# Optimization experiments

Hardware: AMD Instinct MI355X
Metric: run time of the kernel (lower is better)

The kernel has to match this reference:

```python
import jax, jax.numpy as jnp
import numpy as np

EPS = 1e-5
NUM_HEADS = 4


def setup_inputs() -> dict:
    key = jax.random.key(0)
    ks = jax.random.split(key, 6)
    B, C, H, W = 16, 256, 32, 32
    x = jax.random.normal(ks[0], (B, C, H, W), dtype=jnp.float32)
    gamma = jnp.ones((C,), jnp.float32)
    beta = jnp.zeros((C,), jnp.float32)
    run_mean = jax.random.normal(ks[1], (C,), dtype=jnp.float32) * 0.1
    run_var = jax.random.uniform(ks[2], (C,), dtype=jnp.float32, minval=0.5, maxval=1.5)
    qkv_w = jax.random.normal(ks[3], (3 * C, C), dtype=jnp.float32) * (1.0 / np.sqrt(C))
    qkv_b = jnp.zeros((3 * C,), jnp.float32)
    out_w = jax.random.normal(ks[4], (C, C), dtype=jnp.float32) * (1.0 / np.sqrt(C))
    out_b = jnp.zeros((C,), jnp.float32)
    return {"x": x, "gamma": gamma, "beta": beta, "run_mean": run_mean,
            "run_var": run_var, "qkv_w": qkv_w, "qkv_b": qkv_b,
            "out_w": out_w, "out_b": out_b}


def reference(x, gamma, beta, run_mean, run_var, qkv_w, qkv_b, out_w, out_b):
    B, C, H, W = x.shape
    n = NUM_HEADS
    hd = C // n
    # BatchNorm2d (eval mode, running stats)
    inv = jax.lax.rsqrt(run_var + EPS)
    xn = (x - run_mean[:, None, None]) * (inv * gamma)[:, None, None] + beta[:, None, None]
    # 1x1 conv -> QKV: [B, 3C, H, W]
    qkv = jnp.einsum('oc,bchw->bohw', qkv_w, xn) + qkv_b[:, None, None]
    qkv = qkv.reshape(B, n, 3 * hd, H, W)
    q, k, v = qkv[:, :, :hd], qkv[:, :, hd:2 * hd], qkv[:, :, 2 * hd:]
    # full spatial attention; note scale is sqrt(C), per source
    attn = jnp.einsum('bnchw,bncyx->bnhwyx', q, k) / jnp.sqrt(jnp.float32(C))
    attn = jax.nn.softmax(attn.reshape(B, n, H, W, H * W), axis=-1)
    attn = attn.reshape(B, n, H, W, H, W)
    av = jnp.einsum('bnhwyx,bncyx->bnchw', attn, v).reshape(B, C, H, W)
    out = jnp.einsum('oc,bchw->bohw', out_w, av) + out_b[:, None, None]
    return x + out
```

## Files before the change

kernel.cpp:

```cpp
#include <hip/hip_runtime.h>
#include <hip/hip_bf16.h>

__device__ __forceinline__ float bf2f(unsigned short u) {
    return __uint_as_float(((unsigned int)u) << 16);
}
__device__ __forceinline__ unsigned short f2bf(float f) {
    unsigned int u = __float_as_uint(f);
    unsigned int r = (u + 0x7fffu + ((u >> 16) & 1u)) >> 16;
    return (unsigned short)r;
}
__device__ __forceinline__ float ld1(const void* p, long i, bool isf32) {
    return isf32 ? ((const float*)p)[i] : bf2f(((const unsigned short*)p)[i]);
}

typedef __attribute__((ext_vector_type(8))) short bh8;
typedef __attribute__((ext_vector_type(4))) float f32x4;

#define MFMA(a, b, c) __builtin_amdgcn_mfma_f32_16x16x32_bf16(a, b, c, 0, 0, 0)

#define S_TOK 1024
#define C_DIM 256
#define O_QKV 768
#define HD    64
#define NREG  196608
#define QOFF  0
#define KOFF  65536
#define VOFF  131072

__global__ __launch_bounds__(256) void prep_kernel(
    const void* __restrict__ gamma, const void* __restrict__ beta,
    const void* __restrict__ rmean, const void* __restrict__ rvar,
    const void* __restrict__ qkv_w, const void* __restrict__ qkv_b,
    const void* __restrict__ out_w, const void* __restrict__ out_b,
    unsigned short* __restrict__ w1b, float* __restrict__ b1,
    unsigned short* __restrict__ w2b, float* __restrict__ b2,
    int* __restrict__ flg)
{
    const unsigned g0 = *(const unsigned*)gamma;
    const bool isf32 = (g0 == 0x3F800000u);
    const int t   = threadIdx.x;
    const int blk = blockIdx.x;
    if (blk == 0 && t == 0) flg[0] = isf32 ? 1 : 0;
    if (blk < O_QKV) {
        const int c = t, o = blk;
        const float v  = ld1(rvar, c, isf32);
        const float a  = ld1(gamma, c, isf32) * rsqrtf(fmaxf(v, 0.f) + 1e-5f);
        const float sh = ld1(beta, c, isf32) - ld1(rmean, c, isf32) * a;
        const float w  = ld1(qkv_w, (long)o * C_DIM + c, isf32);
        w1b[(size_t)o * C_DIM + c] = f2bf(w * a);
        __shared__ float red[256];
        red[c] = w * sh;
        __syncthreads();
        for (int st = 128; st > 0; st >>= 1) {
            if (c < st) red[c] += red[c + st];
            __syncthreads();
        }
        if (c == 0) b1[o] = ld1(qkv_b, o, isf32) + red[0];
    } else {
        const int c = t, o = blk - O_QKV;
        w2b[(size_t)o * C_DIM + c] = f2bf(ld1(out_w, (long)o * C_DIM + c, isf32));
        if (c == 0) b2[o] = ld1(out_b, o, isf32);
    }
}

__global__ __launch_bounds__(256) void gemm_qkv_kernel(
    const unsigned short* __restrict__ w1b, const float* __restrict__ b1,
    const void* __restrict__ x, unsigned short* __restrict__ qkv,
    int b0, const int* __restrict__ flg)
{
    const bool isf32 = (flg[0] != 0);
    const int s0 = blockIdx.x * 64;
    const int oh = blockIdx.y;
    const int z  = blockIdx.z;
    const int b  = b0 + z;
    const int t  = threadIdx.x;
    const int wave = t >> 6, lane = t & 63;
    const int quad = lane >> 4, l16 = lane & 15;

    __shared__ unsigned short xs[64 * 266];

    const size_t xbase = (size_t)b * C_DIM * S_TOK + s0 + lane;
#pragma unroll 4
    for (int it = 0; it < 64; ++it) {
        const int ci = it * 4 + wave;
        const float v = ld1(x, xbase + (size_t)ci * S_TOK, isf32);
        xs[lane * 266 + ci] = f2bf(v);
    }
    __syncthreads();

#pragma unroll 1
    for (int ot = 0; ot < 6; ++ot) {
        const int o0 = (oh * 6 + ot) * 64;
        const int ow = o0 + wave * 16 + l16;
        bh8 af[8];
#pragma unroll
        for (int kc = 0; kc < 8; ++kc)
            af[kc] = *(const bh8*)&w1b[(size_t)ow * C_DIM + kc * 32 + quad * 8];

        f32x4 acc[4];
#pragma unroll
        for (int nt = 0; nt < 4; ++nt) acc[nt] = (f32x4){0.f, 0.f, 0.f, 0.f};
#pragma unroll
        for (int kc = 0; kc < 8; ++kc) {
#pragma unroll
            for (int nt = 0; nt < 4; ++nt) {
                const bh8 bf = *(const bh8*)&xs[(nt * 16 + l16) * 266 + kc * 32 + quad * 8];
                acc[nt] = MFMA(af[kc], bf, acc[nt]);
            }
        }
        const int n      = o0 / 192;
        const int region = (o0 >> 6) % 3;
        const int och    = wave * 16 + quad * 4;
        float bias_r[4];
#pragma unroll
        for (int r = 0; r < 4; ++r) bias_r[r] = b1[o0 + och + r];
        unsigned short* hb = qkv + (size_t)z * O_QKV * S_TOK + n * NREG;
        if (region < 2) {
            const float sc = (region == 0) ? 0.0625f : 1.0f;
            unsigned short* qb = hb + (region == 0 ? QOFF : KOFF);
#pragma unroll
            for (int nt = 0; nt < 4; ++nt) {
                const int tk = s0 + nt * 16 + l16;
                ushort4 rr;
                rr.x = f2bf((acc[nt][0] + bias_r[0]) * sc);
                rr.y = f2bf((acc[nt][1] + bias_r[1]) * sc);
                rr.z = f2bf((acc[nt][2] + bias_r[2]) * sc);
                rr.w = f2bf((acc[nt][3] + bias_r[3]) * sc);
                *(ushort4*)&qb[(size_t)tk * 64 + och] = rr;
            }
        } else {
            unsigned short* vb = hb + VOFF;
#pragma unroll
            for (int nt = 0; nt < 4; ++nt) {
                const int tk = s0 + nt * 16 + l16;
#pragma unroll
                for (int r = 0; r < 4; ++r)
                    vb[(size_t)(och + r) * S_TOK + tk] = f2bf(acc[nt][r] + bias_r[r]);
            }
        }
    }
}

__global__ __launch_bounds__(256, 4) void attn_mfma_kernel(
    const unsigned short* __restrict__ qkv, unsigned short* __restrict__ avT)
{
    const int n  = blockIdx.x & 3;
    const int z  = blockIdx.x >> 2;
    const int qt = blockIdx.y;
    const int q0 = qt * 64;
    const int t  = threadIdx.x;
    const int wave = t >> 6, lane = t & 63;
    const int quad = lane >> 4, l16 = lane & 15;

    const unsigned short* qtp = qkv + (size_t)z * O_QKV * S_TOK + n * NREG + QOFF;
    const unsigned short* ktp = qtp + KOFF;
    const unsigned short* vcp = qtp + VOFF;

    __shared__ unsigned short p_lds[64 * 72];
    __shared__ float rs_lds[64 * 4];

    bh8 qf[4][2];
#pragma unroll
    for (int qs = 0; qs < 4; ++qs) {
        const size_t qrow = (size_t)(q0 + qs * 16 + l16) * 64;
        qf[qs][0] = *(const bh8*)&qtp[qrow + quad * 8];
        qf[qs][1] = *(const bh8*)&qtp[qrow + 32 + quad * 8];
    }

    f32x4 oacc[4];
#pragma unroll
    for (int i = 0; i < 4; ++i) oacc[i] = (f32x4){0.f, 0.f, 0.f, 0.f};
    float rs[4][4];
#pragma unroll
    for (int qs = 0; qs < 4; ++qs)
#pragma unroll
        for (int r = 0; r < 4; ++r) rs[qs][r] = 0.f;

    for (int chunk = 0; chunk < 16; ++chunk) {
        const int c0 = chunk * 64;
        const size_t krow = (size_t)(c0 + wave * 16 + l16) * 64;
        const bh8 kf0 = *(const bh8*)&ktp[krow + quad * 8];
        const bh8 kf1 = *(const bh8*)&ktp[krow + 32 + quad * 8];
        const size_t vrow = (size_t)(wave * 16 + l16) * S_TOK + c0;
        const bh8 vf0 = *(const bh8*)&vcp[vrow + quad * 8];
        const bh8 vf1 = *(const bh8*)&vcp[vrow + 32 + quad * 8];

        f32x4 sacc[4];
#pragma unroll
        for (int qs = 0; qs < 4; ++qs) {
            f32x4 a = (f32x4){0.f, 0.f, 0.f, 0.f};
            a = MFMA(qf[qs][0], kf0, a);
            a = MFMA(qf[qs][1], kf1, a);
            sacc[qs] = a;
        }
        __syncthreads();
#pragma unroll
        for (int qs = 0; qs < 4; ++qs) {
#pragma unroll
            for (int r = 0; r < 4; ++r) {
                const float p = __expf(sacc[qs][r] - 8.0f);
                rs[qs][r] += p;
                p_lds[(qs * 16 + quad * 4 + r) * 72 + wave * 16 + l16] =
                    (unsigned short)(__float_as_uint(p) >> 16);
            }
        }
        __syncthreads();
#pragma unroll
        for (int qs = 0; qs < 4; ++qs) {
            const bh8 pf0 = *(const bh8*)&p_lds[(qs * 16 + l16) * 72 + quad * 8];
            const bh8 pf1 = *(const bh8*)&p_lds[(qs * 16 + l16) * 72 + 32 + quad * 8];
            oacc[qs] = MFMA(pf0, vf0, oacc[qs]);
            oacc[qs] = MFMA(pf1, vf1, oacc[qs]);
        }
    }
#pragma unroll
    for (int off = 1; off < 16; off <<= 1) {
#pragma unroll
        for (int qs = 0; qs < 4; ++qs)
#pragma unroll
            for (int r = 0; r < 4; ++r) rs[qs][r] += __shfl_xor(rs[qs][r], off);
    }
    if (l16 == 0) {
#pragma unroll
        for (int qs = 0; qs < 4; ++qs)
#pragma unroll
            for (int r = 0; r < 4; ++r)
                rs_lds[(qs * 16 + quad * 4 + r) * 4 + wave] = rs[qs][r];
    }
    __syncthreads();
    const int ch = wave * 16 + l16;
#pragma unroll
    for (int qs = 0; qs < 4; ++qs) {
#pragma unroll
        for (int r = 0; r < 4; ++r) {
            const int q = qs * 16 + quad * 4 + r;
            const float4 rw = *(const float4*)&rs_lds[q * 4];
            const float inv = 1.0f / (rw.x + rw.y + rw.z + rw.w);
            p_lds[q * 72 + ch] = f2bf(oacc[qs][r] * inv);
        }
    }
    __syncthreads();
    const int tok = t >> 2, cq = t & 3;
    const uint4 w0 = *(const uint4*)&p_lds[tok * 72 + cq * 16];
    const uint4 w1 = *(const uint4*)&p_lds[tok * 72 + cq * 16 + 8];
    unsigned short* dst = avT + (((size_t)z << 10) + q0 + tok) * C_DIM + n * HD + cq * 16;
    *(uint4*)dst = w0;
    *(uint4*)(dst + 8) = w1;
}

__global__ __launch_bounds__(256) void gemm_out_kernel(
    const unsigned short* __restrict__ w2b, const float* __restrict__ b2,
    const void* __restrict__ x, const unsigned short* __restrict__ avT,
    void* __restrict__ out, int b0, const int* __restrict__ flg)
{
    const bool isf32 = (flg[0] != 0);
    const int s0 = blockIdx.x * 64;
    const int o0 = blockIdx.y * 64;
    const int z  = blockIdx.z;
    const int b  = b0 + z;
    const int t  = threadIdx.x;
    const int wave = t >> 6, lane = t & 63;
    const int quad = lane >> 4, l16 = lane & 15;

    __shared__ unsigned short vs_lds[64 * 258];

    const unsigned short* ab = avT + (((size_t)z << 10) + s0) * C_DIM;
#pragma unroll
    for (int it = 0; it < 8; ++it) {
        const int idx = it * 256 + t;
        const int tok = idx >> 5, c = (idx & 31) * 8;
        const bh8 v = *(const bh8*)&ab[tok * C_DIM + c];
        const ushort4* vp = (const ushort4*)&v;
        *(ushort4*)&vs_lds[tok * 258 + c]     = vp[0];
        *(ushort4*)&vs_lds[tok * 258 + c + 4] = vp[1];
    }
    const int ow = o0 + wave * 16 + l16;
    bh8 af[8];
#pragma unroll
    for (int kc = 0; kc < 8; ++kc)
        af[kc] = *(const bh8*)&w2b[(size_t)ow * C_DIM + kc * 32 + quad * 8];
    __syncthreads();

    f32x4 acc[4];
#pragma unroll
    for (int nt = 0; nt < 4; ++nt) acc[nt] = (f32x4){0.f, 0.f, 0.f, 0.f};
#pragma unroll
    for (int kc = 0; kc < 8; ++kc) {
#pragma unroll
        for (int nt = 0; nt < 4; ++nt) {
            const bh8 bf = *(const bh8*)&vs_lds[(nt * 16 + l16) * 258 + kc * 32 + quad * 8];
            acc[nt] = MFMA(af[kc], bf, acc[nt]);
        }
    }
    const int obase = o0 + wave * 16 + quad * 4;
    float bias_r[4];
#pragma unroll
    for (int r = 0; r < 4; ++r) bias_r[r] = b2[obase + r];
#pragma unroll
    for (int nt = 0; nt < 4; ++nt) {
        const int tk = s0 + nt * 16 + l16;
#pragma unroll
        for (int r = 0; r < 4; ++r) {
            const size_t base = ((size_t)b * C_DIM + obase + r) * S_TOK + tk;
            if (isf32) {
                ((float*)out)[base] = acc[nt][r] + bias_r[r] + ((const float*)x)[base];
            } else {
                ((unsigned short*)out)[base] =
                    f2bf(acc[nt][r] + bias_r[r] + bf2f(((const unsigned short*)x)[base]));
            }
        }
    }
}

extern "C" void kernel_launch(void* const* d_in, const int* in_sizes, int n_in,
                              void* d_out, int out_size, void* d_ws, size_t ws_size,
                              hipStream_t stream)
{
    const void* x     = d_in[0];
    const void* gamma = d_in[1];
    const void* beta  = d_in[2];
    const void* rmean = d_in[3];
    const void* rvar  = d_in[4];
    const void* qkv_w = d_in[5];
    const void* qkv_b = d_in[6];
    const void* out_w = d_in[7];
    const void* out_b = d_in[8];

    unsigned short* w1b = (unsigned short*)d_ws;
    unsigned short* w2b = w1b + 768 * 256;
    float* b1 = (float*)(w2b + 256 * 256);
    float* b2 = b1 + 768;
    int*   flg = (int*)(b2 + 256);
    const size_t fixed_bytes = (768 * 256 + 256 * 256) * 2 + (768 + 256) * 4 + 16;
    const size_t per_b = (size_t)(768 * 1024 + 256 * 1024) * 2;

    long long avail = (long long)ws_size - (long long)fixed_bytes;
    int G = (avail > 0) ? (int)(avail / (long long)per_b) : 1;
    if (G < 1) G = 1;
    if (G > 16) G = 16;
    if (G > 1) G &= ~1;

    unsigned short* qkv = (unsigned short*)((char*)d_ws + fixed_bytes);
    unsigned short* avT = qkv + (size_t)G * 768 * 1024;

    prep_kernel<<<1024, 256, 0, stream>>>(gamma, beta, rmean, rvar, qkv_w, qkv_b,
                                          out_w, out_b, w1b, b1, w2b, b2, flg);
    for (int b0 = 0; b0 < 16; b0 += G) {
        const int gb = (16 - b0 < G) ? (16 - b0) : G;
        gemm_qkv_kernel<<<dim3(16, 2, gb), 256, 0, stream>>>(w1b, b1, x, qkv, b0, flg);
        attn_mfma_kernel<<<dim3(4 * gb, 16, 1), 256, 0, stream>>>(qkv, avT);
        gemm_out_kernel<<<dim3(16, 4, gb), 256, 0, stream>>>(w2b, b2, x, avT, d_out, b0, flg);
    }
}
```

Before: 172.1 us.

## Write attention output in place over Q, vectorize x staging, prioritize MFMA waves

The attention kernel now writes its normalized output over the Q rows it already consumed, instead of a separate avT buffer. The output GEMM reads from that per-head layout, which drops the extra workspace and may allow a larger batch group per launch. The QKV GEMM now stages x with float4 (or 8-wide bf16) coalesced loads, with a tighter LDS row stride. s_setprio raises wave priority around the MFMA sections of the attention loop. Risks are more LDS bank conflicts from the transposed scalar stores and a dependence on each block reading only its own Q tile before overwriting it.

```diff
diff --git a/kernel.cpp b/kernel.cpp
--- a/kernel.cpp
+++ b/kernel.cpp
@@ -77,14 +77,32 @@
     const int wave = t >> 6, lane = t & 63;
     const int quad = lane >> 4, l16 = lane & 15;
 
-    __shared__ unsigned short xs[64 * 266];
-
-    const size_t xbase = (size_t)b * C_DIM * S_TOK + s0 + lane;
-#pragma unroll 4
-    for (int it = 0; it < 64; ++it) {
-        const int ci = it * 4 + wave;
-        const float v = ld1(x, xbase + (size_t)ci * S_TOK, isf32);
-        xs[lane * 266 + ci] = f2bf(v);
+    __shared__ unsigned short xs[64 * 258];
+
+    if (isf32) {
+        const float* xp = (const float*)x + (size_t)b * C_DIM * S_TOK + s0;
+#pragma unroll
+        for (int it = 0; it < 16; ++it) {
+            const int g  = it * 256 + t;
+            const int ch = g >> 4, tg = (g & 15) * 4;
+            const float4 v = *(const float4*)&xp[(size_t)ch * S_TOK + tg];
+            xs[(tg    ) * 258 + ch] = f2bf(v.x);
+            xs[(tg + 1) * 258 + ch] = f2bf(v.y);
+            xs[(tg + 2) * 258 + ch] = f2bf(v.z);
+            xs[(tg + 3) * 258 + ch] = f2bf(v.w);
+        }
+    } else {
+        const unsigned short* xp = (const unsigned short*)x + (size_t)b * C_DIM * S_TOK + s0;
+#pragma unroll
+        for (int it = 0; it < 8; ++it) {
+            const int g  = it * 256 + t;
+            const int ch = g >> 3, tg = (g & 7) * 8;
+            const bh8 v = *(const bh8*)&xp[(size_t)ch * S_TOK + tg];
+            const unsigned short* vs = (const unsigned short*)&v;
+#pragma unroll
+            for (int j = 0; j < 8; ++j)
+                xs[(tg + j) * 258 + ch] = vs[j];
+        }
     }
     __syncthreads();
 
@@ -104,7 +122,7 @@
         for (int kc = 0; kc < 8; ++kc) {
 #pragma unroll
             for (int nt = 0; nt < 4; ++nt) {
-                const bh8 bf = *(const bh8*)&xs[(nt * 16 + l16) * 266 + kc * 32 + quad * 8];
+                const bh8 bf = *(const bh8*)&xs[(nt * 16 + l16) * 258 + kc * 32 + quad * 8];
                 acc[nt] = MFMA(af[kc], bf, acc[nt]);
             }
         }
@@ -141,8 +159,7 @@
     }
 }
 
-__global__ __launch_bounds__(256, 4) void attn_mfma_kernel(
-    const unsigned short* __restrict__ qkv, unsigned short* __restrict__ avT)
+__global__ __launch_bounds__(256, 4) void attn_mfma_kernel(unsigned short* __restrict__ qkv)
 {
     const int n  = blockIdx.x & 3;
     const int z  = blockIdx.x >> 2;
@@ -152,7 +169,7 @@
     const int wave = t >> 6, lane = t & 63;
     const int quad = lane >> 4, l16 = lane & 15;
 
-    const unsigned short* qtp = qkv + (size_t)z * O_QKV * S_TOK + n * NREG + QOFF;
+    unsigned short* qtp = qkv + (size_t)z * O_QKV * S_TOK + n * NREG + QOFF;
     const unsigned short* ktp = qtp + KOFF;
     const unsigned short* vcp = qtp + VOFF;
 
@@ -186,6 +203,7 @@
         const bh8 vf1 = *(const bh8*)&vcp[vrow + 32 + quad * 8];
 
         f32x4 sacc[4];
+        __builtin_amdgcn_s_setprio(1);
 #pragma unroll
         for (int qs = 0; qs < 4; ++qs) {
             f32x4 a = (f32x4){0.f, 0.f, 0.f, 0.f};
@@ -193,6 +211,7 @@
             a = MFMA(qf[qs][1], kf1, a);
             sacc[qs] = a;
         }
+        __builtin_amdgcn_s_setprio(0);
         __syncthreads();
 #pragma unroll
         for (int qs = 0; qs < 4; ++qs) {
@@ -205,6 +224,7 @@
             }
         }
         __syncthreads();
+        __builtin_amdgcn_s_setprio(1);
 #pragma unroll
         for (int qs = 0; qs < 4; ++qs) {
             const bh8 pf0 = *(const bh8*)&p_lds[(qs * 16 + l16) * 72 + quad * 8];
@@ -212,6 +232,7 @@
             oacc[qs] = MFMA(pf0, vf0, oacc[qs]);
             oacc[qs] = MFMA(pf1, vf1, oacc[qs]);
         }
+        __builtin_amdgcn_s_setprio(0);
     }
 #pragma unroll
     for (int off = 1; off < 16; off <<= 1) {
@@ -243,14 +264,14 @@
     const int tok = t >> 2, cq = t & 3;
     const uint4 w0 = *(const uint4*)&p_lds[tok * 72 + cq * 16];
     const uint4 w1 = *(const uint4*)&p_lds[tok * 72 + cq * 16 + 8];
-    unsigned short* dst = avT + (((size_t)z << 10) + q0 + tok) * C_DIM + n * HD + cq * 16;
+    unsigned short* dst = qtp + (size_t)(q0 + tok) * 64 + cq * 16;
     *(uint4*)dst = w0;
     *(uint4*)(dst + 8) = w1;
 }
 
 __global__ __launch_bounds__(256) void gemm_out_kernel(
     const unsigned short* __restrict__ w2b, const float* __restrict__ b2,
-    const void* __restrict__ x, const unsigned short* __restrict__ avT,
+    const void* __restrict__ x, const unsigned short* __restrict__ qkv,
     void* __restrict__ out, int b0, const int* __restrict__ flg)
 {
     const bool isf32 = (flg[0] != 0);
@@ -264,12 +285,13 @@
 
     __shared__ unsigned short vs_lds[64 * 258];
 
-    const unsigned short* ab = avT + (((size_t)z << 10) + s0) * C_DIM;
+    const unsigned short* hb = qkv + (size_t)z * O_QKV * S_TOK;
 #pragma unroll
     for (int it = 0; it < 8; ++it) {
         const int idx = it * 256 + t;
         const int tok = idx >> 5, c = (idx & 31) * 8;
-        const bh8 v = *(const bh8*)&ab[tok * C_DIM + c];
+        const int hn = c >> 6, coff = c & 63;
+        const bh8 v = *(const bh8*)&hb[(size_t)hn * NREG + (size_t)(s0 + tok) * 64 + coff];
         const ushort4* vp = (const ushort4*)&v;
         *(ushort4*)&vs_lds[tok * 258 + c]     = vp[0];
         *(ushort4*)&vs_lds[tok * 258 + c + 4] = vp[1];
@@ -332,7 +354,7 @@
     float* b2 = b1 + 768;
     int*   flg = (int*)(b2 + 256);
     const size_t fixed_bytes = (768 * 256 + 256 * 256) * 2 + (768 + 256) * 4 + 16;
-    const size_t per_b = (size_t)(768 * 1024 + 256 * 1024) * 2;
+    const size_t per_b = (size_t)768 * 1024 * 2;
 
     long long avail = (long long)ws_size - (long long)fixed_bytes;
     int G = (avail > 0) ? (int)(avail / (long long)per_b) : 1;
@@ -341,14 +363,13 @@
     if (G > 1) G &= ~1;
 
     unsigned short* qkv = (unsigned short*)((char*)d_ws + fixed_bytes);
-    unsigned short* avT = qkv + (size_t)G * 768 * 1024;
 
     prep_kernel<<<1024, 256, 0, stream>>>(gamma, beta, rmean, rvar, qkv_w, qkv_b,
                                           out_w, out_b, w1b, b1, w2b, b2, flg);
     for (int b0 = 0; b0 < 16; b0 += G) {
         const int gb = (16 - b0 < G) ? (16 - b0) : G;
         gemm_qkv_kernel<<<dim3(16, 2, gb), 256, 0, stream>>>(w1b, b1, x, qkv, b0, flg);
-        attn_mfma_kernel<<<dim3(4 * gb, 16, 1), 256, 0, stream>>>(qkv, avT);
-        gemm_out_kernel<<<dim3(16, 4, gb), 256, 0, stream>>>(w2b, b2, x, avT, d_out, b0, flg);
-    }
-}
+        attn_mfma_kernel<<<dim3(4 * gb, 16, 1), 256, 0, stream>>>(qkv);
+        gemm_out_kernel<<<dim3(16, 4, gb), 256, 0, stream>>>(w2b, b2, x, qkv, d_out, b0, flg);
+    }
+}
```

Result: faster. 155.7 us, median of 2 (-9.5%).
